# Optimization experiments

Measured on AMD Instinct MI355X. Metric: run time of the kernel, lower is better.

## Reference

```python
import jax, jax.numpy as jnp
import numpy as np

DIM = 256
HEADS = 8
DIM_HEAD = 64
HIDDEN = HEADS * DIM_HEAD  # 512
SCALE = DIM_HEAD ** -0.5


def setup_inputs() -> dict:
    key = jax.random.key(0)
    k1, k2, k3, k4 = jax.random.split(key, 4)
    x = jax.random.normal(k1, (4, DIM, 2048), dtype=jnp.float32)
    # Conv1d with kernel_size=1 == pointwise linear over channels; store weights as [out, in]
    w_qkv = jax.random.normal(k2, (HIDDEN * 3, DIM), dtype=jnp.float32) * (DIM ** -0.5)
    w_out = jax.random.normal(k3, (DIM, HIDDEN), dtype=jnp.float32) * (HIDDEN ** -0.5)
    b_out = jax.random.normal(k4, (DIM,), dtype=jnp.float32) * 0.01
    return {"x": x, "w_qkv": w_qkv, "w_out": w_out, "b_out": b_out}


def reference(x, w_qkv, w_out, b_out):
    b, c, n = x.shape
    # pointwise conv == channel matmul: [b, 3*hidden, n]
    qkv = jnp.einsum('oc,bcn->bon', w_qkv, x)
    q, k, v = jnp.split(qkv, 3, axis=1)
    # b (h d) n -> b h d n
    reshape = lambda t: t.reshape(b, HEADS, DIM_HEAD, n)
    q, k, v = reshape(q) * SCALE, reshape(k), reshape(v)
    sim = jnp.einsum('bhdi,bhdj->bhij', q, k)          # [b, h, n, n]
    attn = jax.nn.softmax(sim, axis=-1)
    out = jnp.einsum('bhij,bhdj->bhid', attn, v)        # [b, h, n, d]
    # b h n d -> b (h d) n
    out = out.transpose(0, 1, 3, 2).reshape(b, HIDDEN, n)
    return jnp.einsum('oc,bcn->bon', w_out, out) + b_out[None, :, None]
```

## Files before the change

kernel.cpp:

```cpp
#include <hip/hip_runtime.h>
#include <hip/hip_bf16.h>

using f32x4  = __attribute__((ext_vector_type(4))) float;
using f32x16 = __attribute__((ext_vector_type(16))) float;
using bf16x8 = __attribute__((ext_vector_type(8))) short;
using u32x2  = __attribute__((ext_vector_type(2))) unsigned int;
using u32x4  = __attribute__((ext_vector_type(4))) unsigned int;

#define MFMA16(a, b, c) __builtin_amdgcn_mfma_f32_16x16x32_bf16((a), (b), (c), 0, 0, 0)
#define MFMA32(a, b, c) __builtin_amdgcn_mfma_f32_32x32x16_bf16((a), (b), (c), 0, 0, 0)

static __device__ __forceinline__ unsigned short f2bf(float x) {
    unsigned int u = __builtin_bit_cast(unsigned int, x);
    unsigned int r = (u + 0x7fffu + ((u >> 16) & 1u)) >> 16;
    return (unsigned short)r;
}

static __device__ __forceinline__ unsigned int cvtpk_bf16(float a, float b) {
    unsigned int r;
    asm("v_cvt_pk_bf16_f32 %0, %1, %2" : "=v"(r) : "v"(a), "v"(b));
    return r;
}

static __device__ __forceinline__ float exp2_fast(float x) {
#if __has_builtin(__builtin_amdgcn_exp2f)
    return __builtin_amdgcn_exp2f(x);
#else
    return __expf(x * 0.69314718056f);
#endif
}

static __device__ __forceinline__ void plswap(unsigned int& x, unsigned int& y, int hi) {
#if __has_builtin(__builtin_amdgcn_permlane32_swap)
    u32x2 r = __builtin_amdgcn_permlane32_swap(x, y, false, false);
    x = r[0]; y = r[1];
#else
    unsigned int xs = (unsigned int)__shfl_xor((int)x, 32);
    unsigned int ys = (unsigned int)__shfl_xor((int)y, 32);
    unsigned int nx = hi ? ys : x;
    unsigned int ny = hi ? y  : xs;
    x = nx; y = ny;
#endif
}

#define NB 4
#define DIMC 256
#define NN 2048
#define NH 8
#define DH 64
#define HID 512

#define QSCALE 0.18033688f


#define OFF_XT  0u
#define OFF_WQ  4194304u
#define OFF_WO  4980736u
#define OFF_Q   5242880u
#define OFF_K   13631488u
#define OFF_V   22020096u
#define OFF_AO  30408704u

__global__ __launch_bounds__(256) void k_prep(
    const float* __restrict__ x, const float* __restrict__ wqkv,
    const float* __restrict__ wout,
    unsigned short* __restrict__ xt, unsigned short* __restrict__ wq_b,
    unsigned short* __restrict__ wo_b)
{
    int wg = blockIdx.x + 32 * blockIdx.y + 128 * blockIdx.z;
    int tid = wg * 256 + threadIdx.x;
    if (tid < 98304) {
        int o = tid >> 6, c4 = (tid & 63) * 4;
        float4 v = ((const float4*)wqkv)[tid];
        u32x2 pk; pk[0] = cvtpk_bf16(v.x, v.y); pk[1] = cvtpk_bf16(v.z, v.w);
        int rt = o >> 5, rr = o & 31, sub = rr >> 4, l15f = rr & 15;
        int kt = c4 >> 5, l4f = (c4 >> 3) & 3, e = c4 & 7;
        size_t off = (size_t)(((rt * 8 + kt) * 2 + sub)) * 512 + l15f * 32 + l4f * 8 + e;
        *(u32x2*)(wq_b + off) = pk;
    } else {
        int t2 = tid - 98304;
        int o = t2 >> 7, c4 = (t2 & 127) * 4;
        float4 v = ((const float4*)wout)[t2];
        u32x2 pk; pk[0] = cvtpk_bf16(v.x, v.y); pk[1] = cvtpk_bf16(v.z, v.w);
        int rt = o >> 5, rr = o & 31, sub = rr >> 4, l15f = rr & 15;
        int kt = c4 >> 5, l4f = (c4 >> 3) & 3, e = c4 & 7;
        size_t off = (size_t)(((rt * 16 + kt) * 2 + sub)) * 512 + l15f * 32 + l4f * 8 + e;
        *(u32x2*)(wo_b + off) = pk;
    }

    __shared__ unsigned short tile[64][65];
    int nb = blockIdx.x, cb = blockIdx.y, b = blockIdx.z;
    int t = threadIdx.x;
    int tn = t & 63, tg = t >> 6;
    const float* xp = x + ((size_t)(b * DIMC + cb * 64)) * NN + nb * 64;
#pragma unroll
    for (int it = 0; it < 16; ++it) {
        int c = tg * 16 + it;
        tile[c][tn] = f2bf(xp[(size_t)c * NN + tn]);
    }
    __syncthreads();
    unsigned short* xb = xt + (size_t)b * NN * DIMC;
    int C = cb * 64 + tn;
    int kt = C >> 5, l4f = (C >> 3) & 3, e = C & 7;
#pragma unroll
    for (int it = 0; it < 16; ++it) {
        int n = tg * 16 + it;
        int R = nb * 64 + n;
        int rt = R >> 5, rr = R & 31, sub = rr >> 4, l15f = rr & 15;
        xb[(size_t)(((rt * 8 + kt) * 2 + sub)) * 512 + l15f * 32 + l4f * 8 + e] = tile[tn][n];
    }
}

__global__ __launch_bounds__(256) void k_qkv(
    const unsigned short* __restrict__ wq,
    const unsigned short* __restrict__ xt,
    unsigned short* __restrict__ qT, unsigned short* __restrict__ kTt,
    unsigned short* __restrict__ vTt)
{
    int bx = blockIdx.x;
    int nb = blockIdx.y;
    int b  = blockIdx.z;
    int wid = threadIdx.x >> 6;
    int l = threadIdx.x & 63, l15 = l & 15, l4 = l >> 4;
    int o0 = bx * 64, n0 = nb * 64;
    int wr = wid >> 1, wc = wid & 1;
    int lane_off = l15 * 32 + l4 * 8;
    const unsigned short* xb = xt + (size_t)b * NN * DIMC;
    f32x4 acc[2][2] = {};

    if (bx < 16) {
        int rt_a = nb * 2 + wr;
        int rt_b = bx * 2 + wc;
#pragma unroll
        for (int kt = 0; kt < 8; ++kt) {
            const unsigned short* at = xb + (size_t)((rt_a * 8 + kt) * 2) * 512 + lane_off;
            const unsigned short* bt = wq + (size_t)((rt_b * 8 + kt) * 2) * 512 + lane_off;
            bf16x8 a0 = *(const bf16x8*)(at);
            bf16x8 a1 = *(const bf16x8*)(at + 512);
            bf16x8 b0 = *(const bf16x8*)(bt);
            bf16x8 b1 = *(const bf16x8*)(bt + 512);
            acc[0][0] = MFMA16(a0, b0, acc[0][0]);
            acc[0][1] = MFMA16(a0, b1, acc[0][1]);
            acc[1][0] = MFMA16(a1, b0, acc[1][0]);
            acc[1][1] = MFMA16(a1, b1, acc[1][1]);
        }
#pragma unroll
        for (int fm = 0; fm < 2; ++fm)
#pragma unroll
            for (int fn = 0; fn < 2; ++fn) {
                int ocol = o0 + wc * 32 + fn * 16 + l15;
#pragma unroll
                for (int r = 0; r < 4; ++r) {
                    int nrow = n0 + wr * 32 + fm * 16 + l4 * 4 + r;
                    float v = acc[fm][fn][r];
                    if (ocol < HID) {
                        int h = ocol >> 6, d = ocol & 63;
                        qT[(((size_t)(b * NH + h)) * NN + nrow) * DH + d] = f2bf(v * QSCALE);
                    } else {
                        int o2 = ocol - HID;
                        int h = o2 >> 6, d = o2 & 63;
                        int jt = nrow >> 5, li2 = nrow & 31;
                        int ks = d >> 4, hi2 = (d >> 3) & 1, e = d & 7;
                        kTt[((size_t)(b * NH + h) * 64 + jt) * 2048
                            + ks * 512 + hi2 * 256 + li2 * 8 + e] = f2bf(v);
                    }
                }
            }
    } else {
        int rt_a = bx * 2 + wr;
        int rt_b = nb * 2 + wc;
#pragma unroll
        for (int kt = 0; kt < 8; ++kt) {
            const unsigned short* at = wq + (size_t)((rt_a * 8 + kt) * 2) * 512 + lane_off;
            const unsigned short* bt = xb + (size_t)((rt_b * 8 + kt) * 2) * 512 + lane_off;
            bf16x8 a0 = *(const bf16x8*)(at);
            bf16x8 a1 = *(const bf16x8*)(at + 512);
            bf16x8 b0 = *(const bf16x8*)(bt);
            bf16x8 b1 = *(const bf16x8*)(bt + 512);
            acc[0][0] = MFMA16(a0, b0, acc[0][0]);
            acc[0][1] = MFMA16(a0, b1, acc[0][1]);
            acc[1][0] = MFMA16(a1, b0, acc[1][0]);
            acc[1][1] = MFMA16(a1, b1, acc[1][1]);
        }
#pragma unroll
        for (int fm = 0; fm < 2; ++fm)
#pragma unroll
            for (int fn = 0; fn < 2; ++fn)
#pragma unroll
                for (int r = 0; r < 4; ++r) {
                    int orow = o0 + wr * 32 + fm * 16 + l4 * 4 + r;
                    int ncol = n0 + wc * 32 + fn * 16 + l15;
                    int o2 = orow - 1024;
                    int h = o2 >> 6, dd = o2 & 63;
                    int j = ncol;
                    int jt = j >> 5, js = (j >> 4) & 1, hi2 = (j >> 3) & 1, e = j & 7;
                    int dt = dd >> 5, li2 = dd & 31;
                    vTt[((size_t)(b * NH + h) * 64 + jt) * 2048
                        + (dt * 2 + js) * 512 + hi2 * 256 + li2 * 8 + e] = f2bf(acc[fm][fn][r]);
                }
    }
}

__global__ __launch_bounds__(256) void k_attn5(
    const unsigned short* __restrict__ qT, const unsigned short* __restrict__ kTt,
    const unsigned short* __restrict__ vTt, unsigned short* __restrict__ ao)
{
    __shared__ float obuf[2][64][32];
    __shared__ float mlbuf[2][4][32];
    __shared__ unsigned short tb[2][32 * 72];

    int wg = blockIdx.x;
    int xcd = wg & 7;
    int idx = wg >> 3;
    int bh  = xcd * 4 + (idx & 3);
    int ib  = idx >> 2;
    int b = bh >> 3, h = bh & 7;
    int wid = threadIdx.x >> 6;
    int iw = wid & 1, jw = wid >> 1;
    int l = threadIdx.x & 63, li = l & 31, hi = l >> 5;
    int i0 = ib * 64 + iw * 32;

    const unsigned short* qb  = qT + ((size_t)bh * NN) * DH;
    const unsigned short* ktb = kTt + (size_t)bh * 64 * 2048;
    const unsigned short* vtb = vTt + (size_t)bh * 64 * 2048;

    bf16x8 qf[4];
#pragma unroll
    for (int ks = 0; ks < 4; ++ks)
        qf[ks] = *(const bf16x8*)(qb + (size_t)(i0 + li) * DH + ks * 16 + hi * 8);

    f32x16 o0 = {}, o1 = {};
    float m = -1e30f, lsum = 0.f;

    const int jt0 = jw * 32, jt1 = jt0 + 32;

    const unsigned short* kcur = ktb + (size_t)jt0 * 2048;
    bf16x8 kf[4];
#pragma unroll
    for (int ks = 0; ks < 4; ++ks)
        kf[ks] = *(const bf16x8*)(kcur + ks * 512 + l * 8);

    for (int jt = jt0; jt < jt1; ++jt) {
        const unsigned short* vcur = vtb + (size_t)jt * 2048;
        bf16x8 vf[4];
#pragma unroll
        for (int f = 0; f < 4; ++f)
            vf[f] = *(const bf16x8*)(vcur + f * 512 + l * 8);

        f32x16 s = {};
        __builtin_amdgcn_s_setprio(1);
        s = MFMA32(kf[0], qf[0], s);
        s = MFMA32(kf[1], qf[1], s);
        s = MFMA32(kf[2], qf[2], s);
        s = MFMA32(kf[3], qf[3], s);
        __builtin_amdgcn_s_setprio(0);

        kcur += 2048;
        if (jt + 1 < jt1) {
#pragma unroll
            for (int ks = 0; ks < 4; ++ks)
                kf[ks] = *(const bf16x8*)(kcur + ks * 512 + l * 8);
        }

        float t8[8];
#pragma unroll
        for (int q = 0; q < 8; ++q) t8[q] = fmaxf(s[2 * q], s[2 * q + 1]);
        float t4a = fmaxf(t8[0], t8[1]), t4b = fmaxf(t8[2], t8[3]);
        float t4c = fmaxf(t8[4], t8[5]), t4d = fmaxf(t8[6], t8[7]);
        float pmax = fmaxf(fmaxf(t4a, t4b), fmaxf(t4c, t4d));
        {
            unsigned int pu = __builtin_bit_cast(unsigned int, pmax), pv = pu;
            plswap(pu, pv, hi);
            pmax = fmaxf(__builtin_bit_cast(float, pu), __builtin_bit_cast(float, pv));
        }

        if (!__all(pmax - m <= 8.0f)) {
            float mn = fmaxf(m, pmax);
            float alpha = exp2_fast(m - mn);
            m = mn;
            lsum *= alpha;
#pragma unroll
            for (int r = 0; r < 16; ++r) { o0[r] *= alpha; o1[r] *= alpha; }
        }

        float p[16];
#pragma unroll
        for (int r = 0; r < 16; ++r) p[r] = exp2_fast(s[r] - m);
        float u8[8];
#pragma unroll
        for (int q = 0; q < 8; ++q) u8[q] = p[2 * q] + p[2 * q + 1];
        float u4a = u8[0] + u8[1], u4b = u8[2] + u8[3], u4c = u8[4] + u8[5], u4d = u8[6] + u8[7];
        float rsum = (u4a + u4b) + (u4c + u4d);
        {
            unsigned int pu = __builtin_bit_cast(unsigned int, rsum), pv = pu;
            plswap(pu, pv, hi);
            rsum = __builtin_bit_cast(float, pu) + __builtin_bit_cast(float, pv);
        }
        lsum += rsum;

        unsigned int W[8];
#pragma unroll
        for (int q = 0; q < 8; ++q) W[q] = cvtpk_bf16(p[2 * q], p[2 * q + 1]);
        plswap(W[0], W[2], hi); plswap(W[1], W[3], hi);
        plswap(W[4], W[6], hi); plswap(W[5], W[7], hi);
        u32x4 c0; c0[0] = W[0]; c0[1] = W[1]; c0[2] = W[2]; c0[3] = W[3];
        u32x4 c1; c1[0] = W[4]; c1[1] = W[5]; c1[2] = W[6]; c1[3] = W[7];
        bf16x8 pb0 = __builtin_bit_cast(bf16x8, c0);
        bf16x8 pb1 = __builtin_bit_cast(bf16x8, c1);

        __builtin_amdgcn_s_setprio(1);
        o0 = MFMA32(vf[0], pb0, o0);
        o0 = MFMA32(vf[1], pb1, o0);
        o1 = MFMA32(vf[2], pb0, o1);
        o1 = MFMA32(vf[3], pb1, o1);
        __builtin_amdgcn_s_setprio(0);
    }

    mlbuf[0][wid][li] = m;
    mlbuf[1][wid][li] = lsum;
    __syncthreads();
    float mp = mlbuf[0][wid ^ 2][li];
    float lp = mlbuf[1][wid ^ 2][li];
    float mfin = fmaxf(m, mp);
    float aown = exp2_fast(m - mfin);
    float lfin = lsum * aown + lp * exp2_fast(mp - mfin);
#pragma unroll
    for (int r = 0; r < 16; ++r) { o0[r] *= aown; o1[r] *= aown; }

    if (jw == 1) {
        float* ob = &obuf[iw][0][0];
#pragma unroll
        for (int r = 0; r < 16; ++r) {
            int d0a = (r & 3) + 8 * (r >> 2) + 4 * hi;
            ob[d0a * 32 + li]        = o0[r];
            ob[(32 + d0a) * 32 + li] = o1[r];
        }
    }
    __syncthreads();
    if (jw == 0) {
        const float* ob = &obuf[iw][0][0];
#pragma unroll
        for (int r = 0; r < 16; ++r) {
            int d0a = (r & 3) + 8 * (r >> 2) + 4 * hi;
            o0[r] += ob[d0a * 32 + li];
            o1[r] += ob[(32 + d0a) * 32 + li];
        }

        float inv = 1.0f / lfin;
        unsigned short* tw = &tb[iw][0];
#pragma unroll
        for (int dt = 0; dt < 2; ++dt) {
            const f32x16& oo = dt ? o1 : o0;
#pragma unroll
            for (int q = 0; q < 8; ++q) {
                int r = 2 * q;
                int d0 = dt * 32 + (r & 3) + 8 * (r >> 2) + 4 * hi;
                unsigned int wpk = cvtpk_bf16(oo[r] * inv, oo[r + 1] * inv);
                *(unsigned int*)((char*)tw + li * 144 + d0 * 2) = wpk;
            }
        }
        int rt = i0 >> 5;
        unsigned short* pao = ao + (size_t)b * NN * HID
            + (size_t)(((rt * 16 + 2 * h + hi) * 2 + (li >> 4))) * 512 + (li & 15) * 32;
#pragma unroll
        for (int k = 0; k < 4; ++k) {
            bf16x8 v = *(const bf16x8*)((const char*)tw + li * 144 + (hi * 32 + k * 8) * 2);
            *(bf16x8*)(pao + k * 8) = v;
        }
    }
}

__global__ __launch_bounds__(256) void k_proj(
    const unsigned short* __restrict__ wo,
    const unsigned short* __restrict__ ao,
    const float* __restrict__ bout, float* __restrict__ out)
{
    int ob = blockIdx.x, nb = blockIdx.y, b = blockIdx.z;
    int wid = threadIdx.x >> 6;
    int l = threadIdx.x & 63, l15 = l & 15, l4 = l >> 4;
    int wr = wid >> 1, wc = wid & 1;
    int o0 = ob * 64 + wr * 32, n0 = nb * 64 + wc * 32;
    int lane_off = l15 * 32 + l4 * 8;
    int rt_a = ob * 2 + wr;
    int rt_b = nb * 2 + wc;
    const unsigned short* aob = ao + (size_t)b * NN * HID;
    f32x4 acc[2][2] = {};
#pragma unroll
    for (int kt = 0; kt < 16; ++kt) {
        const unsigned short* at = wo + (size_t)((rt_a * 16 + kt) * 2) * 512 + lane_off;
        const unsigned short* bt = aob + (size_t)((rt_b * 16 + kt) * 2) * 512 + lane_off;
        bf16x8 a0 = *(const bf16x8*)(at);
        bf16x8 a1 = *(const bf16x8*)(at + 512);
        bf16x8 b0 = *(const bf16x8*)(bt);
        bf16x8 b1 = *(const bf16x8*)(bt + 512);
        acc[0][0] = MFMA16(a0, b0, acc[0][0]);
        acc[0][1] = MFMA16(a0, b1, acc[0][1]);
        acc[1][0] = MFMA16(a1, b0, acc[1][0]);
        acc[1][1] = MFMA16(a1, b1, acc[1][1]);
    }
#pragma unroll
    for (int fm = 0; fm < 2; ++fm)
#pragma unroll
        for (int fn = 0; fn < 2; ++fn)
#pragma unroll
            for (int r = 0; r < 4; ++r) {
                int o = o0 + fm * 16 + l4 * 4 + r;
                int n = n0 + fn * 16 + l15;
                out[((size_t)(b * DIMC + o)) * NN + n] = acc[fm][fn][r] + bout[o];
            }
}

extern "C" void kernel_launch(void* const* d_in, const int* in_sizes, int n_in,
                              void* d_out, int out_size, void* d_ws, size_t ws_size,
                              hipStream_t stream)
{
    const float* x    = (const float*)d_in[0];
    const float* wqkv = (const float*)d_in[1];
    const float* wout = (const float*)d_in[2];
    const float* bout = (const float*)d_in[3];
    float* out = (float*)d_out;
    char* ws = (char*)d_ws;

    unsigned short* xt  = (unsigned short*)(ws + OFF_XT);
    unsigned short* wqb = (unsigned short*)(ws + OFF_WQ);
    unsigned short* wob = (unsigned short*)(ws + OFF_WO);
    unsigned short* qT  = (unsigned short*)(ws + OFF_Q);
    unsigned short* kTt = (unsigned short*)(ws + OFF_K);
    unsigned short* vTt = (unsigned short*)(ws + OFF_V);
    unsigned short* ao  = (unsigned short*)(ws + OFF_AO);

    hipLaunchKernelGGL(k_prep, dim3(32, 4, 4), dim3(256), 0, stream, x, wqkv, wout, xt, wqb, wob);
    hipLaunchKernelGGL(k_qkv, dim3(24, 32, 4), dim3(256), 0, stream, wqb, xt, qT, kTt, vTt);
    hipLaunchKernelGGL(k_attn5, dim3(1024), dim3(256), 0, stream, qT, kTt, vTt, ao);
    hipLaunchKernelGGL(k_proj, dim3(4, 32, 4), dim3(256), 0, stream, wob, ao, bout, out);
}
```

Baseline: 159.4 us.

## Swap QKV GEMM operand roles so epilogue writes packed bf16 vectors in MFMA-tiled layout

The QKV projection kernel now swaps A/B operands for Q/K blocks (weights as rows, tokens as columns) and x-major for V blocks, so each lane's four accumulator values are contiguous in the destination tiled layout. The epilogue packs them with v_cvt_pk_bf16 into 8-byte stores, replacing scattered 2-byte stores. Q also moves to the same MFMA-fragment tiled layout as K, and the attention kernel loads Q fragments as contiguous 16-byte per-lane loads. This targets store inefficiency in k_qkv and relies on the new index math matching the attention kernel's expected layouts.

```diff
diff --git a/kernel.cpp b/kernel.cpp
--- a/kernel.cpp
+++ b/kernel.cpp
@@ -114,7 +114,7 @@
 __global__ __launch_bounds__(256) void k_qkv(
     const unsigned short* __restrict__ wq,
     const unsigned short* __restrict__ xt,
-    unsigned short* __restrict__ qT, unsigned short* __restrict__ kTt,
+    unsigned short* __restrict__ qTt, unsigned short* __restrict__ kTt,
     unsigned short* __restrict__ vTt)
 {
     int bx = blockIdx.x;
@@ -122,87 +122,65 @@
     int b  = blockIdx.z;
     int wid = threadIdx.x >> 6;
     int l = threadIdx.x & 63, l15 = l & 15, l4 = l >> 4;
-    int o0 = bx * 64, n0 = nb * 64;
     int wr = wid >> 1, wc = wid & 1;
     int lane_off = l15 * 32 + l4 * 8;
     const unsigned short* xb = xt + (size_t)b * NN * DIMC;
+    bool isv = (bx >= 16);
+
+    int rt_a = isv ? (nb * 2 + wr) : (bx * 2 + wr);
+    int rt_b = isv ? (bx * 2 + wc) : (nb * 2 + wc);
+    const unsigned short* abase = isv ? xb : wq;
+    const unsigned short* bbase = isv ? wq : xb;
+
     f32x4 acc[2][2] = {};
-
-    if (bx < 16) {
-        int rt_a = nb * 2 + wr;
-        int rt_b = bx * 2 + wc;
-#pragma unroll
-        for (int kt = 0; kt < 8; ++kt) {
-            const unsigned short* at = xb + (size_t)((rt_a * 8 + kt) * 2) * 512 + lane_off;
-            const unsigned short* bt = wq + (size_t)((rt_b * 8 + kt) * 2) * 512 + lane_off;
-            bf16x8 a0 = *(const bf16x8*)(at);
-            bf16x8 a1 = *(const bf16x8*)(at + 512);
-            bf16x8 b0 = *(const bf16x8*)(bt);
-            bf16x8 b1 = *(const bf16x8*)(bt + 512);
-            acc[0][0] = MFMA16(a0, b0, acc[0][0]);
-            acc[0][1] = MFMA16(a0, b1, acc[0][1]);
-            acc[1][0] = MFMA16(a1, b0, acc[1][0]);
-            acc[1][1] = MFMA16(a1, b1, acc[1][1]);
-        }
+#pragma unroll
+    for (int kt = 0; kt < 8; ++kt) {
+        const unsigned short* at = abase + (size_t)((rt_a * 8 + kt) * 2) * 512 + lane_off;
+        const unsigned short* bt = bbase + (size_t)((rt_b * 8 + kt) * 2) * 512 + lane_off;
+        bf16x8 a0 = *(const bf16x8*)(at);
+        bf16x8 a1 = *(const bf16x8*)(at + 512);
+        bf16x8 b0 = *(const bf16x8*)(bt);
+        bf16x8 b1 = *(const bf16x8*)(bt + 512);
+        acc[0][0] = MFMA16(a0, b0, acc[0][0]);
+        acc[0][1] = MFMA16(a0, b1, acc[0][1]);
+        acc[1][0] = MFMA16(a1, b0, acc[1][0]);
+        acc[1][1] = MFMA16(a1, b1, acc[1][1]);
+    }
+
+    int hi2 = (l4 >> 1), e0 = (l4 & 1) * 4;
+    if (!isv) {
+        int h = (bx < 8) ? bx : (bx - 8);
+        unsigned short* dst = (bx < 8) ? qTt : kTt;
+        float s = (bx < 8) ? QSCALE : 1.0f;
+        size_t hbase = ((size_t)(b * NH + h) * 64 + (nb * 2 + wc)) * 2048;
 #pragma unroll
         for (int fm = 0; fm < 2; ++fm)
 #pragma unroll
             for (int fn = 0; fn < 2; ++fn) {
-                int ocol = o0 + wc * 32 + fn * 16 + l15;
-#pragma unroll
-                for (int r = 0; r < 4; ++r) {
-                    int nrow = n0 + wr * 32 + fm * 16 + l4 * 4 + r;
-                    float v = acc[fm][fn][r];
-                    if (ocol < HID) {
-                        int h = ocol >> 6, d = ocol & 63;
-                        qT[(((size_t)(b * NH + h)) * NN + nrow) * DH + d] = f2bf(v * QSCALE);
-                    } else {
-                        int o2 = ocol - HID;
-                        int h = o2 >> 6, d = o2 & 63;
-                        int jt = nrow >> 5, li2 = nrow & 31;
-                        int ks = d >> 4, hi2 = (d >> 3) & 1, e = d & 7;
-                        kTt[((size_t)(b * NH + h) * 64 + jt) * 2048
-                            + ks * 512 + hi2 * 256 + li2 * 8 + e] = f2bf(v);
-                    }
-                }
+                int li = fn * 16 + l15;
+                u32x2 pk;
+                pk[0] = cvtpk_bf16(acc[fm][fn][0] * s, acc[fm][fn][1] * s);
+                pk[1] = cvtpk_bf16(acc[fm][fn][2] * s, acc[fm][fn][3] * s);
+                *(u32x2*)(dst + hbase + (wr * 2 + fm) * 512 + hi2 * 256 + li * 8 + e0) = pk;
             }
     } else {
-        int rt_a = bx * 2 + wr;
-        int rt_b = nb * 2 + wc;
-#pragma unroll
-        for (int kt = 0; kt < 8; ++kt) {
-            const unsigned short* at = wq + (size_t)((rt_a * 8 + kt) * 2) * 512 + lane_off;
-            const unsigned short* bt = xb + (size_t)((rt_b * 8 + kt) * 2) * 512 + lane_off;
-            bf16x8 a0 = *(const bf16x8*)(at);
-            bf16x8 a1 = *(const bf16x8*)(at + 512);
-            bf16x8 b0 = *(const bf16x8*)(bt);
-            bf16x8 b1 = *(const bf16x8*)(bt + 512);
-            acc[0][0] = MFMA16(a0, b0, acc[0][0]);
-            acc[0][1] = MFMA16(a0, b1, acc[0][1]);
-            acc[1][0] = MFMA16(a1, b0, acc[1][0]);
-            acc[1][1] = MFMA16(a1, b1, acc[1][1]);
-        }
+        int h = bx - 16;
+        size_t hbase = ((size_t)(b * NH + h) * 64 + (nb * 2 + wr)) * 2048;
 #pragma unroll
         for (int fm = 0; fm < 2; ++fm)
 #pragma unroll
-            for (int fn = 0; fn < 2; ++fn)
-#pragma unroll
-                for (int r = 0; r < 4; ++r) {
-                    int orow = o0 + wr * 32 + fm * 16 + l4 * 4 + r;
-                    int ncol = n0 + wc * 32 + fn * 16 + l15;
-                    int o2 = orow - 1024;
-                    int h = o2 >> 6, dd = o2 & 63;
-                    int j = ncol;
-                    int jt = j >> 5, js = (j >> 4) & 1, hi2 = (j >> 3) & 1, e = j & 7;
-                    int dt = dd >> 5, li2 = dd & 31;
-                    vTt[((size_t)(b * NH + h) * 64 + jt) * 2048
-                        + (dt * 2 + js) * 512 + hi2 * 256 + li2 * 8 + e] = f2bf(acc[fm][fn][r]);
-                }
+            for (int fn = 0; fn < 2; ++fn) {
+                int li = fn * 16 + l15;
+                u32x2 pk;
+                pk[0] = cvtpk_bf16(acc[fm][fn][0], acc[fm][fn][1]);
+                pk[1] = cvtpk_bf16(acc[fm][fn][2], acc[fm][fn][3]);
+                *(u32x2*)(vTt + hbase + (wc * 2 + fm) * 512 + hi2 * 256 + li * 8 + e0) = pk;
+            }
     }
 }
 
 __global__ __launch_bounds__(256) void k_attn5(
-    const unsigned short* __restrict__ qT, const unsigned short* __restrict__ kTt,
+    const unsigned short* __restrict__ qTt, const unsigned short* __restrict__ kTt,
     const unsigned short* __restrict__ vTt, unsigned short* __restrict__ ao)
 {
     __shared__ float obuf[2][64][32];
@@ -220,14 +198,14 @@
     int l = threadIdx.x & 63, li = l & 31, hi = l >> 5;
     int i0 = ib * 64 + iw * 32;
 
-    const unsigned short* qb  = qT + ((size_t)bh * NN) * DH;
+    const unsigned short* qtile = qTt + ((size_t)bh * 64 + (ib * 2 + iw)) * 2048;
     const unsigned short* ktb = kTt + (size_t)bh * 64 * 2048;
     const unsigned short* vtb = vTt + (size_t)bh * 64 * 2048;
 
     bf16x8 qf[4];
 #pragma unroll
     for (int ks = 0; ks < 4; ++ks)
-        qf[ks] = *(const bf16x8*)(qb + (size_t)(i0 + li) * DH + ks * 16 + hi * 8);
+        qf[ks] = *(const bf16x8*)(qtile + ks * 512 + l * 8);
 
     f32x16 o0 = {}, o1 = {};
     float m = -1e30f, lsum = 0.f;
@@ -424,13 +402,13 @@
     unsigned short* xt  = (unsigned short*)(ws + OFF_XT);
     unsigned short* wqb = (unsigned short*)(ws + OFF_WQ);
     unsigned short* wob = (unsigned short*)(ws + OFF_WO);
-    unsigned short* qT  = (unsigned short*)(ws + OFF_Q);
+    unsigned short* qTt = (unsigned short*)(ws + OFF_Q);
     unsigned short* kTt = (unsigned short*)(ws + OFF_K);
     unsigned short* vTt = (unsigned short*)(ws + OFF_V);
     unsigned short* ao  = (unsigned short*)(ws + OFF_AO);
 
     hipLaunchKernelGGL(k_prep, dim3(32, 4, 4), dim3(256), 0, stream, x, wqkv, wout, xt, wqb, wob);
-    hipLaunchKernelGGL(k_qkv, dim3(24, 32, 4), dim3(256), 0, stream, wqb, xt, qT, kTt, vTt);
-    hipLaunchKernelGGL(k_attn5, dim3(1024), dim3(256), 0, stream, qT, kTt, vTt, ao);
+    hipLaunchKernelGGL(k_qkv, dim3(24, 32, 4), dim3(256), 0, stream, wqb, xt, qTt, kTt, vTt);
+    hipLaunchKernelGGL(k_attn5, dim3(1024), dim3(256), 0, stream, qTt, kTt, vTt, ao);
     hipLaunchKernelGGL(k_proj, dim3(4, 32, 4), dim3(256), 0, stream, wob, ao, bout, out);
 }
```

Measured after the change: 156.2 us. 2.0% less time.
